# Kernel optimization log

Hardware: AMD Instinct MI355X
Metric: run time of the kernel (lower is better)

Reference implementation:

```python
import jax, jax.numpy as jnp
import numpy as np

D_MODEL = 1024
NUM_HEADS = 16
D_HEAD = D_MODEL // NUM_HEADS


def setup_inputs() -> dict:
    key = jax.random.key(0)
    ks = jax.random.split(key, 12)
    B, S = 4, 2048
    scale = 1.0 / np.sqrt(D_MODEL)
    inp = {
        "query": jax.random.normal(ks[0], (B, S, D_MODEL), dtype=jnp.float32),
        "key": jax.random.normal(ks[1], (B, S, D_MODEL), dtype=jnp.float32),
        "value": jax.random.normal(ks[2], (B, S, D_MODEL), dtype=jnp.float32),
        "Wq": jax.random.normal(ks[3], (D_MODEL, D_MODEL), dtype=jnp.float32) * scale,
        "bq": jnp.zeros((D_MODEL,), dtype=jnp.float32),
        "Wk": jax.random.normal(ks[4], (D_MODEL, D_MODEL), dtype=jnp.float32) * scale,
        "bk": jnp.zeros((D_MODEL,), dtype=jnp.float32),
        "Wv": jax.random.normal(ks[5], (D_MODEL, D_MODEL), dtype=jnp.float32) * scale,
        "bv": jnp.zeros((D_MODEL,), dtype=jnp.float32),
        "Wo": jax.random.normal(ks[6], (D_MODEL, D_MODEL), dtype=jnp.float32) * scale,
        "bo": jnp.zeros((D_MODEL,), dtype=jnp.float32),
    }
    return inp


def reference(query, key, value, Wq, bq, Wk, bk, Wv, bv, Wo, bo):
    B, S, _ = query.shape
    # Linear projections (torch Linear: x @ W.T + b), split into heads: [B, H, S, Dh]
    Q = (query @ Wq.T + bq).reshape(B, S, NUM_HEADS, D_HEAD).transpose(0, 2, 1, 3)
    K = (key @ Wk.T + bk).reshape(B, S, NUM_HEADS, D_HEAD).transpose(0, 2, 1, 3)
    V = (value @ Wv.T + bv).reshape(B, S, NUM_HEADS, D_HEAD).transpose(0, 2, 1, 3)
    scores = jnp.einsum("bhqd,bhkd->bhqk", Q, K) / np.sqrt(D_HEAD).astype(np.float32)
    attn = jax.nn.softmax(scores, axis=-1)  # dropout is identity in eval mode
    out = jnp.einsum("bhqk,bhkd->bhqd", attn, V)
    out = out.transpose(0, 2, 1, 3).reshape(B, S, D_MODEL)
    out = out @ Wo.T + bo
    avg_attention = attn.mean(axis=1)  # [B, S, S]
    return (out, avg_attention)
```

## Files before the change

kernel.cpp:

```cpp
#include <hip/hip_runtime.h>
#include <hip/hip_bf16.h>


#define DEVI __device__ __forceinline__

typedef __attribute__((ext_vector_type(8))) short bf16x8;
typedef __attribute__((ext_vector_type(4))) short bf16x4;
typedef __attribute__((ext_vector_type(4))) float f32x4;

#define MFMA_BF16(a, b, c) __builtin_amdgcn_mfma_f32_16x16x32_bf16(a, b, c, 0, 0, 0)

constexpr int Bn = 4;
constexpr int Sn = 2048;
constexpr int Dn = 1024;
constexpr int Hn = 16;

DEVI unsigned short f2bf_rn(float x) {
    unsigned u = __float_as_uint(x);
    u += 0x7fffu + ((u >> 16) & 1u);
    return (unsigned short)(u >> 16);
}
DEVI float bf2f(unsigned short h) { return __uint_as_float(((unsigned)h) << 16); }

DEVI int swz32(int r, int k) { return r * 32 + ((((k >> 3) ^ r) & 3) << 3) + (k & 7); }
DEVI int swz64(int r, int k) { return r * 64 + ((((k >> 3) ^ r) & 7) << 3) + (k & 7); }

__global__ __launch_bounds__(256) void cvt_plain3(
    const float* __restrict__ a, const float* __restrict__ b, const float* __restrict__ c,
    unsigned short* __restrict__ oa, unsigned short* __restrict__ ob,
    unsigned short* __restrict__ oc)
{
    const float* s = blockIdx.y == 0 ? a : blockIdx.y == 1 ? b : c;
    unsigned short* d = blockIdx.y == 0 ? oa : blockIdx.y == 1 ? ob : oc;
    const size_t i = ((size_t)blockIdx.x * 256 + threadIdx.x) * 8;
    const float4 v0 = *reinterpret_cast<const float4*>(s + i);
    const float4 v1 = *reinterpret_cast<const float4*>(s + i + 4);
    const float* p0 = reinterpret_cast<const float*>(&v0);
    const float* p1 = reinterpret_cast<const float*>(&v1);
    bf16x8 o;
#pragma unroll
    for (int j = 0; j < 4; ++j) {
        o[j] = (short)f2bf_rn(p0[j]);
        o[4 + j] = (short)f2bf_rn(p1[j]);
    }
    *reinterpret_cast<bf16x8*>(d + i) = o;
}

__global__ __launch_bounds__(256) void cvt_split4(
    const float* __restrict__ w0, const float* __restrict__ w1,
    const float* __restrict__ w2, const float* __restrict__ w3,
    unsigned short* __restrict__ h0, unsigned short* __restrict__ l0,
    unsigned short* __restrict__ h1, unsigned short* __restrict__ l1,
    unsigned short* __restrict__ h2, unsigned short* __restrict__ l2,
    unsigned short* __restrict__ h3, unsigned short* __restrict__ l3)
{
    const int y = blockIdx.y;
    const float* s = y == 0 ? w0 : y == 1 ? w1 : y == 2 ? w2 : w3;
    unsigned short* dh = y == 0 ? h0 : y == 1 ? h1 : y == 2 ? h2 : h3;
    unsigned short* dl = y == 0 ? l0 : y == 1 ? l1 : y == 2 ? l2 : l3;
    const size_t i = ((size_t)blockIdx.x * 256 + threadIdx.x) * 8;
    const float4 v0 = *reinterpret_cast<const float4*>(s + i);
    const float4 v1 = *reinterpret_cast<const float4*>(s + i + 4);
    const float* p0 = reinterpret_cast<const float*>(&v0);
    const float* p1 = reinterpret_cast<const float*>(&v1);
    bf16x8 oh, ol;
#pragma unroll
    for (int j = 0; j < 4; ++j) {
        unsigned short h = f2bf_rn(p0[j]);
        oh[j] = (short)h;
        ol[j] = (short)f2bf_rn(p0[j] - bf2f(h));
        h = f2bf_rn(p1[j]);
        oh[4 + j] = (short)h;
        ol[4 + j] = (short)f2bf_rn(p1[j] - bf2f(h));
    }
    *reinterpret_cast<bf16x8*>(dh + i) = oh;
    *reinterpret_cast<bf16x8*>(dl + i) = ol;
}

template <int MODE>
__global__ __launch_bounds__(256) void gemm_bf(
    const unsigned short* __restrict__ Xbf,
    const unsigned short* __restrict__ Whi, const unsigned short* __restrict__ Wlo,
    const float* __restrict__ bias,
    unsigned short* __restrict__ o_bf, float* __restrict__ o_f32)
{
    constexpr int K = Dn;
    __shared__ __align__(16) unsigned short sA[128 * 32];
    __shared__ __align__(16) unsigned short sBh[128 * 32];
    __shared__ __align__(16) unsigned short sBl[128 * 32];

    const int tid = threadIdx.x, lane = tid & 63, w = tid >> 6;
    const int row0 = blockIdx.y * 128, col0 = blockIdx.x * 128;
    const int wm = (w >> 1) * 64, wn = (w & 1) * 64;
    const int fr = lane & 15, kof = (lane >> 4) * 8;

    f32x4 acc[4][4] = {};

    for (int k0 = 0; k0 < K; k0 += 32) {
#pragma unroll
        for (int j = 0; j < 2; ++j) {
            const int v = tid + j * 256;
            const int r = v >> 2, c8 = (v & 3) * 8;
            const int ia = swz32(r, c8);
            *(bf16x8*)&sA[ia] = *(const bf16x8*)(Xbf + (size_t)(row0 + r) * K + k0 + c8);
            *(bf16x8*)&sBh[ia] = *(const bf16x8*)(Whi + (size_t)(col0 + r) * K + k0 + c8);
            *(bf16x8*)&sBl[ia] = *(const bf16x8*)(Wlo + (size_t)(col0 + r) * K + k0 + c8);
        }
        __syncthreads();

        bf16x8 fa[4], fbh[4], fbl[4];
#pragma unroll
        for (int m = 0; m < 4; ++m) fa[m] = *(const bf16x8*)&sA[swz32(wm + m * 16 + fr, kof)];
#pragma unroll
        for (int n = 0; n < 4; ++n) {
            const int ib = swz32(wn + n * 16 + fr, kof);
            fbh[n] = *(const bf16x8*)&sBh[ib];
            fbl[n] = *(const bf16x8*)&sBl[ib];
        }
#pragma unroll
        for (int m = 0; m < 4; ++m)
#pragma unroll
            for (int n = 0; n < 4; ++n) {
                acc[m][n] = MFMA_BF16(fa[m], fbh[n], acc[m][n]);
                acc[m][n] = MFMA_BF16(fa[m], fbl[n], acc[m][n]);
            }
        __syncthreads();
    }

    float bv_[4];
#pragma unroll
    for (int n = 0; n < 4; ++n) bv_[n] = bias[col0 + wn + n * 16 + fr];

#pragma unroll
    for (int m = 0; m < 4; ++m)
#pragma unroll
        for (int n = 0; n < 4; ++n)
#pragma unroll
            for (int r = 0; r < 4; ++r) {
                const int row = row0 + wm + m * 16 + (lane >> 4) * 4 + r;
                const int col = col0 + wn + n * 16 + fr;
                const float v = acc[m][n][r] + bv_[n];
                if (MODE == 0) {
                    const int bb = row >> 11, s = row & 2047;
                    const int hh = col >> 6, dh = col & 63;
                    o_bf[((size_t)(bb * Hn + hh) * Sn + s) * 64 + dh] = f2bf_rn(v);
                } else if (MODE == 1) {
                    const int bb = row >> 11, s = row & 2047;
                    const int hh = col >> 6, dh = col & 63;
                    o_bf[((size_t)(bb * Hn + hh) * 64 + dh) * Sn + s] = f2bf_rn(v);
                } else {
                    o_f32[(size_t)row * Dn + col] = v;
                }
            }
}

__global__ __launch_bounds__(256) void flash_fwd(
    const unsigned short* __restrict__ Qbf, const unsigned short* __restrict__ Kbf,
    const unsigned short* __restrict__ Vt,
    unsigned short* __restrict__ attn_bf, float* __restrict__ m_ws, float* __restrict__ l_ws)
{
    __shared__ __align__(16) unsigned short kh_l[64 * 64];
    __shared__ __align__(16) unsigned short vt_l[64 * 64];
    __shared__ __align__(16) unsigned short p_l[4 * 16 * 64];

    const int tid = threadIdx.x, lane = tid & 63, w = tid >> 6;
    const int qt = blockIdx.x & 31;
    const int h = (blockIdx.x >> 5) & 15;
    const int b = blockIdx.x >> 9;
    const int fr = lane & 15, kof = (lane >> 4) * 8;
    const size_t head = (size_t)(b * Hn + h) * Sn;
    const int qbase = qt * 64;
    const int qrow = qbase + w * 16 + fr;

    bf16x8 aq[2];
    {
        const unsigned short* qp = Qbf + (head + qrow) * 64;
        aq[0] = *(const bf16x8*)(qp + kof);
        aq[1] = *(const bf16x8*)(qp + 32 + kof);
    }

    float m_r[4] = {-1e30f, -1e30f, -1e30f, -1e30f};
    float l_r[4] = {0.f, 0.f, 0.f, 0.f};
    f32x4 o[4] = {};

    for (int kb = 0; kb < Sn; kb += 64) {
#pragma unroll
        for (int j = 0; j < 2; ++j) {
            const int u = tid + j * 256;
            const int r = u >> 3, sg = (u & 7) * 8;
            *(bf16x8*)&kh_l[swz64(r, sg)] = *(const bf16x8*)(Kbf + (head + kb + r) * 64 + sg);
            *(bf16x8*)&vt_l[swz64(r, sg)] =
                *(const bf16x8*)(Vt + ((size_t)(b * Hn + h) * 64 + r) * Sn + kb + sg);
        }
        __syncthreads();

        f32x4 sc[4] = {};
#pragma unroll
        for (int n = 0; n < 4; ++n) {
            const int kr = n * 16 + fr;
#pragma unroll
            for (int ks = 0; ks < 2; ++ks) {
                const bf16x8 bh = *(const bf16x8*)&kh_l[swz64(kr, ks * 32 + kof)];
                sc[n] = MFMA_BF16(aq[ks], bh, sc[n]);
            }
        }
#pragma unroll
        for (int n = 0; n < 4; ++n) sc[n] *= 0.125f;

        float mnew[4];
        bool grow = false;
#pragma unroll
        for (int r = 0; r < 4; ++r) {
            float rm = fmaxf(fmaxf(sc[0][r], sc[1][r]), fmaxf(sc[2][r], sc[3][r]));
            rm = fmaxf(rm, __shfl_xor(rm, 1));
            rm = fmaxf(rm, __shfl_xor(rm, 2));
            rm = fmaxf(rm, __shfl_xor(rm, 4));
            rm = fmaxf(rm, __shfl_xor(rm, 8));
            mnew[r] = fmaxf(m_r[r], rm);
            grow = grow || (mnew[r] > m_r[r]);
        }
        if (__any((int)grow)) {
#pragma unroll
            for (int r = 0; r < 4; ++r) {
                const float scale_ = __expf(m_r[r] - mnew[r]);
#pragma unroll
                for (int n = 0; n < 4; ++n) o[n][r] *= scale_;
                l_r[r] *= scale_;
                m_r[r] = mnew[r];
            }
        }

        float rsum[4] = {0.f, 0.f, 0.f, 0.f};
#pragma unroll
        for (int n = 0; n < 4; ++n)
#pragma unroll
            for (int r = 0; r < 4; ++r) {
                const float p = __expf(sc[n][r] - m_r[r]);
                rsum[r] += p;
                p_l[w * 1024 + swz64((lane >> 4) * 4 + r, n * 16 + fr)] = f2bf_rn(p);
            }
#pragma unroll
        for (int r = 0; r < 4; ++r) {
            float t = rsum[r];
            t += __shfl_xor(t, 1);
            t += __shfl_xor(t, 2);
            t += __shfl_xor(t, 4);
            t += __shfl_xor(t, 8);
            l_r[r] += t;
        }

        const bf16x8 pa0 = *(const bf16x8*)&p_l[w * 1024 + swz64(fr, kof)];
        const bf16x8 pa1 = *(const bf16x8*)&p_l[w * 1024 + swz64(fr, 32 + kof)];
#pragma unroll
        for (int n = 0; n < 4; ++n) {
            const bf16x8 bv0 = *(const bf16x8*)&vt_l[swz64(n * 16 + fr, kof)];
            const bf16x8 bv1 = *(const bf16x8*)&vt_l[swz64(n * 16 + fr, 32 + kof)];
            o[n] = MFMA_BF16(pa0, bv0, o[n]);
            o[n] = MFMA_BF16(pa1, bv1, o[n]);
        }
        __syncthreads();
    }

#pragma unroll
    for (int r = 0; r < 4; ++r) {
        const float inv = 1.f / l_r[r];
        const int row_ = qbase + w * 16 + (lane >> 4) * 4 + r;
#pragma unroll
        for (int n = 0; n < 4; ++n)
            attn_bf[((size_t)(b * Sn + row_)) * Dn + h * 64 + n * 16 + fr] =
                f2bf_rn(o[n][r] * inv);
    }
    if (fr == 0) {
#pragma unroll
        for (int r = 0; r < 4; ++r) {
            const int row_ = qbase + w * 16 + (lane >> 4) * 4 + r;
            m_ws[head + row_] = m_r[r];
            l_ws[head + row_] = l_r[r];
        }
    }
}

__global__ __launch_bounds__(256) void avg_attn_kernel(
    const unsigned short* __restrict__ Qbf, const unsigned short* __restrict__ Kbf,
    const float* __restrict__ m_ws, const float* __restrict__ l_ws,
    float* __restrict__ avg)
{
    __shared__ __align__(16) unsigned short kh_l[64 * 64];

    const int tid = threadIdx.x, lane = tid & 63, w = tid >> 6;
    const int kt = blockIdx.x & 31;
    const int qt = (blockIdx.x >> 5) & 31;
    const int b = blockIdx.x >> 10;
    const int fr = lane & 15, kof = (lane >> 4) * 8;
    const int qbase = qt * 64, kbase = kt * 64;
    const int qrow = qbase + w * 16 + fr;

    f32x4 facc[4] = {};

    for (int h = 0; h < Hn; ++h) {
        const size_t head = (size_t)(b * Hn + h) * Sn;
#pragma unroll
        for (int j = 0; j < 2; ++j) {
            const int u = tid + j * 256;
            const int r = u >> 3, sg = (u & 7) * 8;
            *(bf16x8*)&kh_l[swz64(r, sg)] = *(const bf16x8*)(Kbf + (head + kbase + r) * 64 + sg);
        }
        __syncthreads();

        const unsigned short* qp = Qbf + (head + qrow) * 64;
        const bf16x8 aq0 = *(const bf16x8*)(qp + kof);
        const bf16x8 aq1 = *(const bf16x8*)(qp + 32 + kof);

        f32x4 sc[4] = {};
#pragma unroll
        for (int n = 0; n < 4; ++n) {
            const int kr = n * 16 + fr;
            const bf16x8 bh0 = *(const bf16x8*)&kh_l[swz64(kr, kof)];
            const bf16x8 bh1 = *(const bf16x8*)&kh_l[swz64(kr, 32 + kof)];
            sc[n] = MFMA_BF16(aq0, bh0, sc[n]);
            sc[n] = MFMA_BF16(aq1, bh1, sc[n]);
        }
#pragma unroll
        for (int r = 0; r < 4; ++r) {
            const int row_ = qbase + w * 16 + (lane >> 4) * 4 + r;
            const float mm = m_ws[head + row_];
            const float li = 0.0625f / l_ws[head + row_];
#pragma unroll
            for (int n = 0; n < 4; ++n) {
                const float ss = sc[n][r] * 0.125f;
                facc[n][r] += __expf(ss - mm) * li;
            }
        }
        __syncthreads();
    }

#pragma unroll
    for (int r = 0; r < 4; ++r) {
        const int row_ = qbase + w * 16 + (lane >> 4) * 4 + r;
#pragma unroll
        for (int n = 0; n < 4; ++n)
            avg[((size_t)(b * Sn + row_)) * Sn + kbase + n * 16 + fr] = facc[n][r];
    }
}

extern "C" void kernel_launch(void* const* d_in, const int* in_sizes, int n_in,
                              void* d_out, int out_size, void* d_ws, size_t ws_size,
                              hipStream_t stream)
{
    const float* query = (const float*)d_in[0];
    const float* key_ = (const float*)d_in[1];
    const float* value = (const float*)d_in[2];
    const float* Wq = (const float*)d_in[3];
    const float* bq = (const float*)d_in[4];
    const float* Wk = (const float*)d_in[5];
    const float* bk = (const float*)d_in[6];
    const float* Wv = (const float*)d_in[7];
    const float* bv = (const float*)d_in[8];
    const float* Wo = (const float*)d_in[9];
    const float* bo = (const float*)d_in[10];

    const size_t QE = (size_t)Bn * Hn * Sn * 64;
    const size_t WE = (size_t)Dn * Dn;

    unsigned short* Qbf = (unsigned short*)d_ws;
    unsigned short* Kbf = Qbf + QE;
    unsigned short* Vt = Kbf + QE;
    unsigned short* Xq = Vt + QE;
    unsigned short* Xk = Xq + QE;
    unsigned short* Xv = Xk + QE;
    unsigned short* Wqh = Xv + QE;
    unsigned short* Wql = Wqh + WE;
    unsigned short* Wkh = Wql + WE;
    unsigned short* Wkl = Wkh + WE;
    unsigned short* Wvh = Wkl + WE;
    unsigned short* Wvl = Wvh + WE;
    unsigned short* Woh = Wvl + WE;
    unsigned short* Wol = Woh + WE;
    float* m_ws = (float*)(Wol + WE);
    float* l_ws = m_ws + (size_t)Bn * Hn * Sn;
    unsigned short* attn_bf = Xq;

    float* out0 = (float*)d_out;
    float* avg = out0 + (size_t)Bn * Sn * Dn;

    cvt_plain3<<<dim3(4096, 3), 256, 0, stream>>>(query, key_, value, Xq, Xk, Xv);
    cvt_split4<<<dim3(512, 4), 256, 0, stream>>>(Wq, Wk, Wv, Wo, Wqh, Wql, Wkh, Wkl,
                                                 Wvh, Wvl, Woh, Wol);

    const dim3 gg(8, 64), bb(256);
    gemm_bf<0><<<gg, bb, 0, stream>>>(Xq, Wqh, Wql, bq, Qbf, nullptr);
    gemm_bf<0><<<gg, bb, 0, stream>>>(Xk, Wkh, Wkl, bk, Kbf, nullptr);
    gemm_bf<1><<<gg, bb, 0, stream>>>(Xv, Wvh, Wvl, bv, Vt, nullptr);
    flash_fwd<<<dim3(Bn * Hn * (Sn / 64)), bb, 0, stream>>>(Qbf, Kbf, Vt, attn_bf,
                                                            m_ws, l_ws);
    avg_attn_kernel<<<dim3(Bn * 32 * 32), bb, 0, stream>>>(Qbf, Kbf, m_ws, l_ws, avg);
    gemm_bf<2><<<gg, bb, 0, stream>>>(attn_bf, Woh, Wol, bo, nullptr, out0);
}
```

Before: 687.3 us.

## Use direct global-to-LDS loads and 64x128 tiles in projection GEMMs

The projection GEMM now loads tiles with global_load_lds, writing straight from global memory into shared memory with a pre-swizzled source address instead of staging through registers. The block tile shrinks from 128x128 to 64x128 and each wave owns a 64x32 slice, which doubles the grid. The aim is to cut register pressure and VGPR round trips and to raise occupancy for the four GEMMs. The cost is lower per-block reuse of the weight tiles. It also adds an unused oscale parameter, always passed as 1.0.

```diff
diff --git a/kernel.cpp b/kernel.cpp
--- a/kernel.cpp
+++ b/kernel.cpp
@@ -5,7 +5,6 @@
 #define DEVI __device__ __forceinline__
 
 typedef __attribute__((ext_vector_type(8))) short bf16x8;
-typedef __attribute__((ext_vector_type(4))) short bf16x4;
 typedef __attribute__((ext_vector_type(4))) float f32x4;
 
 #define MFMA_BF16(a, b, c) __builtin_amdgcn_mfma_f32_16x16x32_bf16(a, b, c, 0, 0, 0)
@@ -24,6 +23,12 @@
 
 DEVI int swz32(int r, int k) { return r * 32 + ((((k >> 3) ^ r) & 3) << 3) + (k & 7); }
 DEVI int swz64(int r, int k) { return r * 64 + ((((k >> 3) ^ r) & 7) << 3) + (k & 7); }
+
+DEVI void gload16(const unsigned short* g, unsigned short* l) {
+    __builtin_amdgcn_global_load_lds(
+        (const __attribute__((address_space(1))) unsigned int*)g,
+        (__attribute__((address_space(3))) unsigned int*)l, 16, 0, 0);
+}
 
 __global__ __launch_bounds__(256) void cvt_plain3(
     const float* __restrict__ a, const float* __restrict__ b, const float* __restrict__ c,
@@ -81,38 +86,46 @@
 __global__ __launch_bounds__(256) void gemm_bf(
     const unsigned short* __restrict__ Xbf,
     const unsigned short* __restrict__ Whi, const unsigned short* __restrict__ Wlo,
-    const float* __restrict__ bias,
+    const float* __restrict__ bias, float oscale,
     unsigned short* __restrict__ o_bf, float* __restrict__ o_f32)
 {
     constexpr int K = Dn;
-    __shared__ __align__(16) unsigned short sA[128 * 32];
+    __shared__ __align__(16) unsigned short sA[64 * 32];
     __shared__ __align__(16) unsigned short sBh[128 * 32];
     __shared__ __align__(16) unsigned short sBl[128 * 32];
 
     const int tid = threadIdx.x, lane = tid & 63, w = tid >> 6;
-    const int row0 = blockIdx.y * 128, col0 = blockIdx.x * 128;
-    const int wm = (w >> 1) * 64, wn = (w & 1) * 64;
-    const int fr = lane & 15, kof = (lane >> 4) * 8;
-
-    f32x4 acc[4][4] = {};
+    const int row0 = blockIdx.y * 64, col0 = blockIdx.x * 128;
+    const int wn = w * 32;
+    const int fr = lane & 15, hi = lane >> 4, kof = hi * 8;
+
+    const int gA = w * 64 + lane;
+    const int rA = gA >> 2, cA = ((gA & 3) ^ rA) & 3;
+    const int gB0 = w * 64 + lane, gB1 = 256 + w * 64 + lane;
+    const int rB0 = gB0 >> 2, cB0 = ((gB0 & 3) ^ rB0) & 3;
+    const int rB1 = gB1 >> 2, cB1 = ((gB1 & 3) ^ rB1) & 3;
+
+    const unsigned short* pa = Xbf + (size_t)(row0 + rA) * K + cA * 8;
+    const unsigned short* pb0h = Whi + (size_t)(col0 + rB0) * K + cB0 * 8;
+    const unsigned short* pb1h = Whi + (size_t)(col0 + rB1) * K + cB1 * 8;
+    const unsigned short* pb0l = Wlo + (size_t)(col0 + rB0) * K + cB0 * 8;
+    const unsigned short* pb1l = Wlo + (size_t)(col0 + rB1) * K + cB1 * 8;
+
+    f32x4 acc[4][2] = {};
 
     for (int k0 = 0; k0 < K; k0 += 32) {
-#pragma unroll
-        for (int j = 0; j < 2; ++j) {
-            const int v = tid + j * 256;
-            const int r = v >> 2, c8 = (v & 3) * 8;
-            const int ia = swz32(r, c8);
-            *(bf16x8*)&sA[ia] = *(const bf16x8*)(Xbf + (size_t)(row0 + r) * K + k0 + c8);
-            *(bf16x8*)&sBh[ia] = *(const bf16x8*)(Whi + (size_t)(col0 + r) * K + k0 + c8);
-            *(bf16x8*)&sBl[ia] = *(const bf16x8*)(Wlo + (size_t)(col0 + r) * K + k0 + c8);
-        }
-        __syncthreads();
-
-        bf16x8 fa[4], fbh[4], fbl[4];
-#pragma unroll
-        for (int m = 0; m < 4; ++m) fa[m] = *(const bf16x8*)&sA[swz32(wm + m * 16 + fr, kof)];
-#pragma unroll
-        for (int n = 0; n < 4; ++n) {
+        gload16(pa + k0, &sA[(w * 64) * 8]);
+        gload16(pb0h + k0, &sBh[(w * 64) * 8]);
+        gload16(pb1h + k0, &sBh[(256 + w * 64) * 8]);
+        gload16(pb0l + k0, &sBl[(w * 64) * 8]);
+        gload16(pb1l + k0, &sBl[(256 + w * 64) * 8]);
+        __syncthreads();
+
+        bf16x8 fa[4], fbh[2], fbl[2];
+#pragma unroll
+        for (int m = 0; m < 4; ++m) fa[m] = *(const bf16x8*)&sA[swz32(m * 16 + fr, kof)];
+#pragma unroll
+        for (int n = 0; n < 2; ++n) {
             const int ib = swz32(wn + n * 16 + fr, kof);
             fbh[n] = *(const bf16x8*)&sBh[ib];
             fbl[n] = *(const bf16x8*)&sBl[ib];
@@ -120,27 +133,28 @@
 #pragma unroll
         for (int m = 0; m < 4; ++m)
 #pragma unroll
-            for (int n = 0; n < 4; ++n) {
+            for (int n = 0; n < 2; ++n) {
                 acc[m][n] = MFMA_BF16(fa[m], fbh[n], acc[m][n]);
                 acc[m][n] = MFMA_BF16(fa[m], fbl[n], acc[m][n]);
             }
         __syncthreads();
     }
 
-    float bv_[4];
-#pragma unroll
-    for (int n = 0; n < 4; ++n) bv_[n] = bias[col0 + wn + n * 16 + fr];
+    float bv_[2];
+#pragma unroll
+    for (int n = 0; n < 2; ++n) bv_[n] = bias[col0 + wn + n * 16 + fr];
 
 #pragma unroll
     for (int m = 0; m < 4; ++m)
 #pragma unroll
-        for (int n = 0; n < 4; ++n)
+        for (int n = 0; n < 2; ++n)
 #pragma unroll
             for (int r = 0; r < 4; ++r) {
-                const int row = row0 + wm + m * 16 + (lane >> 4) * 4 + r;
+                const int row = row0 + m * 16 + hi * 4 + r;
                 const int col = col0 + wn + n * 16 + fr;
-                const float v = acc[m][n][r] + bv_[n];
+                float v = acc[m][n][r] + bv_[n];
                 if (MODE == 0) {
+                    v *= oscale;
                     const int bb = row >> 11, s = row & 2047;
                     const int hh = col >> 6, dh = col & 63;
                     o_bf[((size_t)(bb * Hn + hh) * Sn + s) * 64 + dh] = f2bf_rn(v);
@@ -387,12 +401,12 @@
     cvt_split4<<<dim3(512, 4), 256, 0, stream>>>(Wq, Wk, Wv, Wo, Wqh, Wql, Wkh, Wkl,
                                                  Wvh, Wvl, Woh, Wol);
 
-    const dim3 gg(8, 64), bb(256);
-    gemm_bf<0><<<gg, bb, 0, stream>>>(Xq, Wqh, Wql, bq, Qbf, nullptr);
-    gemm_bf<0><<<gg, bb, 0, stream>>>(Xk, Wkh, Wkl, bk, Kbf, nullptr);
-    gemm_bf<1><<<gg, bb, 0, stream>>>(Xv, Wvh, Wvl, bv, Vt, nullptr);
+    const dim3 gg(8, 128), bb(256);
+    gemm_bf<0><<<gg, bb, 0, stream>>>(Xq, Wqh, Wql, bq, 1.0f, Qbf, nullptr);
+    gemm_bf<0><<<gg, bb, 0, stream>>>(Xk, Wkh, Wkl, bk, 1.0f, Kbf, nullptr);
+    gemm_bf<1><<<gg, bb, 0, stream>>>(Xv, Wvh, Wvl, bv, 1.0f, Vt, nullptr);
     flash_fwd<<<dim3(Bn * Hn * (Sn / 64)), bb, 0, stream>>>(Qbf, Kbf, Vt, attn_bf,
                                                             m_ws, l_ws);
     avg_attn_kernel<<<dim3(Bn * 32 * 32), bb, 0, stream>>>(Qbf, Kbf, m_ws, l_ws, avg);
-    gemm_bf<2><<<gg, bb, 0, stream>>>(attn_bf, Woh, Wol, bo, nullptr, out0);
-}
+    gemm_bf<2><<<gg, bb, 0, stream>>>(attn_bf, Woh, Wol, bo, 1.0f, nullptr, out0);
+}
```

Measured after the change: 728.0 us. 5.9% more time.

## Use direct global-to-LDS loads, double-buffer flash K/V, fold softmax scale into Q

Applied to the files above, without the earlier changes.

Replaces register-staged global-to-shared copies in the GEMM, flash and avg-attention kernels with the global_load_lds builtin, using a pre-swizzled source address per lane. The flash kernel gets double-buffered K/V tiles so the next tile's load overlaps compute on the current one. The 1/sqrt(d) scale and log2(e) are folded into the Q projection epilogue, so the softmax uses exp2 and skips a per-element multiply. This adds LDS use for the double buffers and relies on the async LDS load ordering being correct with the existing barriers; the m/l statistics now live in base-2 units.

```diff
diff --git a/kernel.cpp b/kernel.cpp
--- a/kernel.cpp
+++ b/kernel.cpp
@@ -5,7 +5,6 @@
 #define DEVI __device__ __forceinline__
 
 typedef __attribute__((ext_vector_type(8))) short bf16x8;
-typedef __attribute__((ext_vector_type(4))) short bf16x4;
 typedef __attribute__((ext_vector_type(4))) float f32x4;
 
 #define MFMA_BF16(a, b, c) __builtin_amdgcn_mfma_f32_16x16x32_bf16(a, b, c, 0, 0, 0)
@@ -24,6 +23,12 @@
 
 DEVI int swz32(int r, int k) { return r * 32 + ((((k >> 3) ^ r) & 3) << 3) + (k & 7); }
 DEVI int swz64(int r, int k) { return r * 64 + ((((k >> 3) ^ r) & 7) << 3) + (k & 7); }
+
+DEVI void gload16(const unsigned short* g, unsigned short* l) {
+    __builtin_amdgcn_global_load_lds(
+        (const __attribute__((address_space(1))) unsigned int*)g,
+        (__attribute__((address_space(3))) unsigned int*)l, 16, 0, 0);
+}
 
 __global__ __launch_bounds__(256) void cvt_plain3(
     const float* __restrict__ a, const float* __restrict__ b, const float* __restrict__ c,
@@ -81,7 +86,7 @@
 __global__ __launch_bounds__(256) void gemm_bf(
     const unsigned short* __restrict__ Xbf,
     const unsigned short* __restrict__ Whi, const unsigned short* __restrict__ Wlo,
-    const float* __restrict__ bias,
+    const float* __restrict__ bias, float oscale,
     unsigned short* __restrict__ o_bf, float* __restrict__ o_f32)
 {
     constexpr int K = Dn;
@@ -92,20 +97,28 @@
     const int tid = threadIdx.x, lane = tid & 63, w = tid >> 6;
     const int row0 = blockIdx.y * 128, col0 = blockIdx.x * 128;
     const int wm = (w >> 1) * 64, wn = (w & 1) * 64;
-    const int fr = lane & 15, kof = (lane >> 4) * 8;
+    const int fr = lane & 15, hi = lane >> 4, kof = hi * 8;
+
+    const int g0 = tid, g1 = tid + 256;
+    const int r0 = g0 >> 2, c0 = ((g0 & 3) ^ r0) & 3;
+    const int r1 = g1 >> 2, c1 = ((g1 & 3) ^ r1) & 3;
+
+    const unsigned short* pa0 = Xbf + (size_t)(row0 + r0) * K + c0 * 8;
+    const unsigned short* pa1 = Xbf + (size_t)(row0 + r1) * K + c1 * 8;
+    const unsigned short* pbh0 = Whi + (size_t)(col0 + r0) * K + c0 * 8;
+    const unsigned short* pbh1 = Whi + (size_t)(col0 + r1) * K + c1 * 8;
+    const unsigned short* pbl0 = Wlo + (size_t)(col0 + r0) * K + c0 * 8;
+    const unsigned short* pbl1 = Wlo + (size_t)(col0 + r1) * K + c1 * 8;
 
     f32x4 acc[4][4] = {};
 
     for (int k0 = 0; k0 < K; k0 += 32) {
-#pragma unroll
-        for (int j = 0; j < 2; ++j) {
-            const int v = tid + j * 256;
-            const int r = v >> 2, c8 = (v & 3) * 8;
-            const int ia = swz32(r, c8);
-            *(bf16x8*)&sA[ia] = *(const bf16x8*)(Xbf + (size_t)(row0 + r) * K + k0 + c8);
-            *(bf16x8*)&sBh[ia] = *(const bf16x8*)(Whi + (size_t)(col0 + r) * K + k0 + c8);
-            *(bf16x8*)&sBl[ia] = *(const bf16x8*)(Wlo + (size_t)(col0 + r) * K + k0 + c8);
-        }
+        gload16(pa0 + k0, &sA[(w * 64) * 8]);
+        gload16(pa1 + k0, &sA[(256 + w * 64) * 8]);
+        gload16(pbh0 + k0, &sBh[(w * 64) * 8]);
+        gload16(pbh1 + k0, &sBh[(256 + w * 64) * 8]);
+        gload16(pbl0 + k0, &sBl[(w * 64) * 8]);
+        gload16(pbl1 + k0, &sBl[(256 + w * 64) * 8]);
         __syncthreads();
 
         bf16x8 fa[4], fbh[4], fbl[4];
@@ -137,10 +150,11 @@
         for (int n = 0; n < 4; ++n)
 #pragma unroll
             for (int r = 0; r < 4; ++r) {
-                const int row = row0 + wm + m * 16 + (lane >> 4) * 4 + r;
+                const int row = row0 + wm + m * 16 + hi * 4 + r;
                 const int col = col0 + wn + n * 16 + fr;
-                const float v = acc[m][n][r] + bv_[n];
+                float v = acc[m][n][r] + bv_[n];
                 if (MODE == 0) {
+                    v *= oscale;
                     const int bb = row >> 11, s = row & 2047;
                     const int hh = col >> 6, dh = col & 63;
                     o_bf[((size_t)(bb * Hn + hh) * Sn + s) * 64 + dh] = f2bf_rn(v);
@@ -159,8 +173,8 @@
     const unsigned short* __restrict__ Vt,
     unsigned short* __restrict__ attn_bf, float* __restrict__ m_ws, float* __restrict__ l_ws)
 {
-    __shared__ __align__(16) unsigned short kh_l[64 * 64];
-    __shared__ __align__(16) unsigned short vt_l[64 * 64];
+    __shared__ __align__(16) unsigned short kh_l[2][64 * 64];
+    __shared__ __align__(16) unsigned short vt_l[2][64 * 64];
     __shared__ __align__(16) unsigned short p_l[4 * 16 * 64];
 
     const int tid = threadIdx.x, lane = tid & 63, w = tid >> 6;
@@ -172,6 +186,14 @@
     const int qbase = qt * 64;
     const int qrow = qbase + w * 16 + fr;
 
+    const int gS0 = w * 64 + lane, gS1 = 256 + w * 64 + lane;
+    const int rS0 = gS0 >> 3, cS0 = ((gS0 & 7) ^ rS0) & 7;
+    const int rS1 = gS1 >> 3, cS1 = ((gS1 & 7) ^ rS1) & 7;
+    const unsigned short* kp0 = Kbf + (head + rS0) * 64 + cS0 * 8;
+    const unsigned short* kp1 = Kbf + (head + rS1) * 64 + cS1 * 8;
+    const unsigned short* vp0 = Vt + ((size_t)(b * Hn + h) * 64 + rS0) * Sn + cS0 * 8;
+    const unsigned short* vp1 = Vt + ((size_t)(b * Hn + h) * 64 + rS1) * Sn + cS1 * 8;
+
     bf16x8 aq[2];
     {
         const unsigned short* qp = Qbf + (head + qrow) * 64;
@@ -182,17 +204,22 @@
     float m_r[4] = {-1e30f, -1e30f, -1e30f, -1e30f};
     float l_r[4] = {0.f, 0.f, 0.f, 0.f};
     f32x4 o[4] = {};
+    int cur = 0;
+
+    gload16(kp0, &kh_l[0][(w * 64) * 8]);
+    gload16(kp1, &kh_l[0][(256 + w * 64) * 8]);
+    gload16(vp0, &vt_l[0][(w * 64) * 8]);
+    gload16(vp1, &vt_l[0][(256 + w * 64) * 8]);
+    __syncthreads();
 
     for (int kb = 0; kb < Sn; kb += 64) {
-#pragma unroll
-        for (int j = 0; j < 2; ++j) {
-            const int u = tid + j * 256;
-            const int r = u >> 3, sg = (u & 7) * 8;
-            *(bf16x8*)&kh_l[swz64(r, sg)] = *(const bf16x8*)(Kbf + (head + kb + r) * 64 + sg);
-            *(bf16x8*)&vt_l[swz64(r, sg)] =
-                *(const bf16x8*)(Vt + ((size_t)(b * Hn + h) * 64 + r) * Sn + kb + sg);
-        }
-        __syncthreads();
+        if (kb + 64 < Sn) {
+            const int nb = cur ^ 1;
+            gload16(kp0 + (size_t)(kb + 64) * 64, &kh_l[nb][(w * 64) * 8]);
+            gload16(kp1 + (size_t)(kb + 64) * 64, &kh_l[nb][(256 + w * 64) * 8]);
+            gload16(vp0 + kb + 64, &vt_l[nb][(w * 64) * 8]);
+            gload16(vp1 + kb + 64, &vt_l[nb][(256 + w * 64) * 8]);
+        }
 
         f32x4 sc[4] = {};
 #pragma unroll
@@ -200,12 +227,10 @@
             const int kr = n * 16 + fr;
 #pragma unroll
             for (int ks = 0; ks < 2; ++ks) {
-                const bf16x8 bh = *(const bf16x8*)&kh_l[swz64(kr, ks * 32 + kof)];
+                const bf16x8 bh = *(const bf16x8*)&kh_l[cur][swz64(kr, ks * 32 + kof)];
                 sc[n] = MFMA_BF16(aq[ks], bh, sc[n]);
             }
         }
-#pragma unroll
-        for (int n = 0; n < 4; ++n) sc[n] *= 0.125f;
 
         float mnew[4];
         bool grow = false;
@@ -222,7 +247,7 @@
         if (__any((int)grow)) {
 #pragma unroll
             for (int r = 0; r < 4; ++r) {
-                const float scale_ = __expf(m_r[r] - mnew[r]);
+                const float scale_ = __builtin_amdgcn_exp2f(m_r[r] - mnew[r]);
 #pragma unroll
                 for (int n = 0; n < 4; ++n) o[n][r] *= scale_;
                 l_r[r] *= scale_;
@@ -235,7 +260,7 @@
         for (int n = 0; n < 4; ++n)
 #pragma unroll
             for (int r = 0; r < 4; ++r) {
-                const float p = __expf(sc[n][r] - m_r[r]);
+                const float p = __builtin_amdgcn_exp2f(sc[n][r] - m_r[r]);
                 rsum[r] += p;
                 p_l[w * 1024 + swz64((lane >> 4) * 4 + r, n * 16 + fr)] = f2bf_rn(p);
             }
@@ -253,12 +278,13 @@
         const bf16x8 pa1 = *(const bf16x8*)&p_l[w * 1024 + swz64(fr, 32 + kof)];
 #pragma unroll
         for (int n = 0; n < 4; ++n) {
-            const bf16x8 bv0 = *(const bf16x8*)&vt_l[swz64(n * 16 + fr, kof)];
-            const bf16x8 bv1 = *(const bf16x8*)&vt_l[swz64(n * 16 + fr, 32 + kof)];
+            const bf16x8 bv0 = *(const bf16x8*)&vt_l[cur][swz64(n * 16 + fr, kof)];
+            const bf16x8 bv1 = *(const bf16x8*)&vt_l[cur][swz64(n * 16 + fr, 32 + kof)];
             o[n] = MFMA_BF16(pa0, bv0, o[n]);
             o[n] = MFMA_BF16(pa1, bv1, o[n]);
         }
         __syncthreads();
+        cur ^= 1;
     }
 
 #pragma unroll
@@ -295,16 +321,16 @@
     const int qbase = qt * 64, kbase = kt * 64;
     const int qrow = qbase + w * 16 + fr;
 
+    const int gS0 = w * 64 + lane, gS1 = 256 + w * 64 + lane;
+    const int rS0 = gS0 >> 3, cS0 = ((gS0 & 7) ^ rS0) & 7;
+    const int rS1 = gS1 >> 3, cS1 = ((gS1 & 7) ^ rS1) & 7;
+
     f32x4 facc[4] = {};
 
     for (int h = 0; h < Hn; ++h) {
         const size_t head = (size_t)(b * Hn + h) * Sn;
-#pragma unroll
-        for (int j = 0; j < 2; ++j) {
-            const int u = tid + j * 256;
-            const int r = u >> 3, sg = (u & 7) * 8;
-            *(bf16x8*)&kh_l[swz64(r, sg)] = *(const bf16x8*)(Kbf + (head + kbase + r) * 64 + sg);
-        }
+        gload16(Kbf + (head + kbase + rS0) * 64 + cS0 * 8, &kh_l[(w * 64) * 8]);
+        gload16(Kbf + (head + kbase + rS1) * 64 + cS1 * 8, &kh_l[(256 + w * 64) * 8]);
         __syncthreads();
 
         const unsigned short* qp = Qbf + (head + qrow) * 64;
@@ -326,10 +352,8 @@
             const float mm = m_ws[head + row_];
             const float li = 0.0625f / l_ws[head + row_];
 #pragma unroll
-            for (int n = 0; n < 4; ++n) {
-                const float ss = sc[n][r] * 0.125f;
-                facc[n][r] += __expf(ss - mm) * li;
-            }
+            for (int n = 0; n < 4; ++n)
+                facc[n][r] += __builtin_amdgcn_exp2f(sc[n][r] - mm) * li;
         }
         __syncthreads();
     }
@@ -383,16 +407,18 @@
     float* out0 = (float*)d_out;
     float* avg = out0 + (size_t)Bn * Sn * Dn;
 
+    const float QSC = 0.125f * 1.44269504088896341f;
+
     cvt_plain3<<<dim3(4096, 3), 256, 0, stream>>>(query, key_, value, Xq, Xk, Xv);
     cvt_split4<<<dim3(512, 4), 256, 0, stream>>>(Wq, Wk, Wv, Wo, Wqh, Wql, Wkh, Wkl,
                                                  Wvh, Wvl, Woh, Wol);
 
     const dim3 gg(8, 64), bb(256);
-    gemm_bf<0><<<gg, bb, 0, stream>>>(Xq, Wqh, Wql, bq, Qbf, nullptr);
-    gemm_bf<0><<<gg, bb, 0, stream>>>(Xk, Wkh, Wkl, bk, Kbf, nullptr);
-    gemm_bf<1><<<gg, bb, 0, stream>>>(Xv, Wvh, Wvl, bv, Vt, nullptr);
+    gemm_bf<0><<<gg, bb, 0, stream>>>(Xq, Wqh, Wql, bq, QSC, Qbf, nullptr);
+    gemm_bf<0><<<gg, bb, 0, stream>>>(Xk, Wkh, Wkl, bk, 1.0f, Kbf, nullptr);
+    gemm_bf<1><<<gg, bb, 0, stream>>>(Xv, Wvh, Wvl, bv, 1.0f, Vt, nullptr);
     flash_fwd<<<dim3(Bn * Hn * (Sn / 64)), bb, 0, stream>>>(Qbf, Kbf, Vt, attn_bf,
                                                             m_ws, l_ws);
     avg_attn_kernel<<<dim3(Bn * 32 * 32), bb, 0, stream>>>(Qbf, Kbf, m_ws, l_ws, avg);
-    gemm_bf<2><<<gg, bb, 0, stream>>>(attn_bf, Woh, Wol, bo, nullptr, out0);
-}
+    gemm_bf<2><<<gg, bb, 0, stream>>>(attn_bf, Woh, Wol, bo, 1.0f, nullptr, out0);
+}
```

New measurement: 662.8 us. 3.6% less time.
